# Performance work log

Hardware: AMD Instinct MI355X
Metric: run time of the kernel (lower is better)

## Reference

```python
import jax, jax.numpy as jnp
import numpy as np
from jax import lax

# ---- config (mirrors UpFIRDnConv2d(in=64,out=64,k=3,stride=1,jit=False), in_size=128) ----
B, C_IN, C_OUT, K = 8, 64, 64, 3
IN_SIZE = 128
LRELU_UP = 2          # lrelu_upsampling
FILTER_SIZE = 6
UP = 2                # up_factor = ceil(max(in,out)*2/in) = 2 (out_size == in_size)
DN = 2                # dn_factor = 2
GAIN = float(np.sqrt(2.0))
SLOPE = 0.2


def _firwin_lowpass(numtaps, cutoff, width, fs):
    """Replicates scipy.signal.firwin(numtaps, cutoff, width=width, fs=fs) for lowpass."""
    nyq = fs / 2.0
    c = cutoff / nyq            # normalized cutoff (~0.99995)
    w = width / nyq             # normalized transition width (2.0)
    # kaiser_atten / kaiser_beta (scipy formulas)
    atten = 2.285 * (numtaps - 1) * np.pi * w + 7.95
    if atten > 50:
        beta = 0.1102 * (atten - 8.7)
    elif atten > 21:
        beta = 0.5842 * (atten - 21) ** 0.4 + 0.07886 * (atten - 21)
    else:
        beta = 0.0
    m = np.arange(numtaps) - (numtaps - 1) / 2.0
    h = c * np.sinc(c * m) * np.kaiser(numtaps, beta)
    h = h / h.sum()             # scale=True at f=0
    return h.astype(np.float32)


def setup_inputs() -> dict:
    key = jax.random.key(0)
    k1, k2, k3 = jax.random.split(key, 3)
    x = jax.random.normal(k1, (B, C_IN, IN_SIZE, IN_SIZE), dtype=jnp.float32)
    # Conv2d(64,64,3) params (kaiming-ish scale: 1/sqrt(fan_in))
    fan_in = C_IN * K * K
    conv_w = jax.random.normal(k2, (C_OUT, C_IN, K, K), dtype=jnp.float32) / np.sqrt(fan_in)
    conv_b = jax.random.normal(k3, (C_OUT,), dtype=jnp.float32) * 0.01
    # UpFIRDn2d bias initialized to zeros (reset_parameters)
    bias = jnp.zeros((1, C_OUT, 1, 1), dtype=jnp.float32)
    # FIR filters from firwin (in_size == out_size == 128 here)
    uptaps = FILTER_SIZE * UP   # 12
    dntaps = FILTER_SIZE * DN   # 12
    up1d = _firwin_lowpass(uptaps, IN_SIZE / 2.0001, IN_SIZE, IN_SIZE)
    dn1d = _firwin_lowpass(dntaps, IN_SIZE / 2.0001, IN_SIZE, IN_SIZE)
    up_filter = jnp.asarray(np.outer(up1d, up1d)[None, None], dtype=jnp.float32)  # (1,1,12,12)
    dn_filter = jnp.asarray(np.outer(dn1d, dn1d)[None, None], dtype=jnp.float32)
    return {"x": x, "conv_w": conv_w, "conv_b": conv_b, "bias": bias,
            "up_filter": up_filter, "dn_filter": dn_filter}


def _conv_same(z, w):
    # torch padding='same': total = k-1, left = total//2, extra on the right
    kh, kw = w.shape[-2], w.shape[-1]
    lo_h, lo_w = (kh - 1) // 2, (kw - 1) // 2
    pad = [(lo_h, kh - 1 - lo_h), (lo_w, kw - 1 - lo_w)]
    return lax.conv_general_dilated(z, w, window_strides=(1, 1), padding=pad,
                                    dimension_numbers=("NCHW", "OIHW", "NCHW"))


def reference(x, conv_w, conv_b, bias, up_filter, dn_filter):
    # main 3x3 conv, stride 1, 'same'
    y = _conv_same(x, conv_w) + conv_b[None, :, None, None]
    # UpFIRDn2d
    y = y + bias                                   # (B, C, H, W)
    b, c, h, w = y.shape
    y = y.reshape(b * c, 1, h, w)
    y = jnp.repeat(jnp.repeat(y, UP, axis=2), UP, axis=3)   # nearest upsample -> (BC,1,2H,2W)
    y = _conv_same(y, up_filter)                   # 12x12 FIR, 'same'
    y = jnp.where(y >= 0, y, SLOPE * y) * jnp.float32(GAIN) # leaky_relu * gain
    y = _conv_same(y, dn_filter)                   # 12x12 FIR, 'same'
    y = y[:, :, ::DN, ::DN]                        # grid pool
    return y.reshape(b, c, y.shape[-2], y.shape[-1])
```

## Files before the change

kernel.cpp:

```cpp
#include <hip/hip_runtime.h>
#include <hip/hip_bf16.h>
#include <math.h>

#define NB 8
#define CH 64
#define IN_SZ 128
#define PLANE (IN_SZ*IN_SZ)

typedef __attribute__((ext_vector_type(8))) short short8;
typedef __attribute__((ext_vector_type(4))) float f32x4;
typedef __attribute__((ext_vector_type(4))) int   int4v;

#define Y0B   (NB*CH*PLANE*4)
#define WHB   (9*64*64*2)


__device__ __forceinline__ short8 dpp_shift_p1(short8 a, short8 nb) {
  int4v ai = __builtin_bit_cast(int4v, a);
  int4v ni = __builtin_bit_cast(int4v, nb);
  int4v r;
#pragma unroll
  for (int t = 0; t < 4; ++t) {
    int m = __builtin_amdgcn_update_dpp(0, ai[t], 0x101, 0xf, 0xf, true);
    int n = __builtin_amdgcn_update_dpp(0, ni[t], 0x11F, 0xf, 0xf, true);
    r[t] = m | n;
  }
  return __builtin_bit_cast(short8, r);
}
__device__ __forceinline__ short8 dpp_shift_m1(short8 a, short8 nb) {
  int4v ai = __builtin_bit_cast(int4v, a);
  int4v ni = __builtin_bit_cast(int4v, nb);
  int4v r;
#pragma unroll
  for (int t = 0; t < 4; ++t) {
    int m = __builtin_amdgcn_update_dpp(0, ai[t], 0x111, 0xf, 0xf, true);
    int n = __builtin_amdgcn_update_dpp(0, ni[t], 0x10F, 0xf, 0xf, true);
    r[t] = m | n;
  }
  return __builtin_bit_cast(short8, r);
}

__global__ __launch_bounds__(256) void prep_w_kernel(
    const float* __restrict__ w,
    const float* __restrict__ cb,
    const float* __restrict__ bias,
    const float* __restrict__ up2,
    const float* __restrict__ dn2,
    __hip_bfloat16* __restrict__ whi,
    __hip_bfloat16* __restrict__ wlo,
    float* __restrict__ bsum,
    float* __restrict__ f1d) {
  int t = blockIdx.x * 256 + threadIdx.x;
  if (t < 9*64*64) {
    int e   = t & 7;
    int l16 = (t >> 3) & 15;
    int g   = (t >> 7) & 3;
    int ct  = (t >> 9) & 3;
    int cih = (t >> 11) & 1;
    int tap = t >> 12;
    int co = ct*16 + l16;
    int ci = cih*32 + g*8 + e;
    int ky = tap / 3, kx = tap % 3;
    float v = w[((co*64 + ci)*3 + ky)*3 + kx];
    __hip_bfloat16 h = __float2bfloat16(v);
    whi[t] = h;
    wlo[t] = __float2bfloat16(v - __bfloat162float(h));
  }
  if (blockIdx.x == 0) {
    int tid = threadIdx.x;
    if (tid < 64) bsum[tid] = cb[tid] + bias[tid];
    float us = sqrtf(up2[5*12 + 5]);
    float ds = sqrtf(dn2[5*12 + 5]);
    if (tid >= 64 && tid < 70) {
      int j = tid - 64;
      f1d[j] = (up2[(2*j)*12 + 5] + up2[(2*j + 1)*12 + 5]) / us;
    } else if (tid >= 70 && tid < 77) {
      int j = tid - 70;
      float v;
      if (j == 0)      v = up2[0*12 + 5];
      else if (j == 6) v = up2[11*12 + 5];
      else             v = up2[(2*j - 1)*12 + 5] + up2[(2*j)*12 + 5];
      f1d[6 + j] = v / us;
    } else if (tid >= 77 && tid < 89) {
      int k = tid - 77;
      f1d[13 + k] = dn2[k*12 + 5] / ds;
    }
  }
}

__global__ __launch_bounds__(256) void prep_x_kernel(
    const float* __restrict__ x,
    __hip_bfloat16* __restrict__ xhi,
    __hip_bfloat16* __restrict__ xlo) {
  __shared__ float tile[64][129];
  int blk = blockIdx.x;
  int y = blk & 127;
  int b = blk >> 7;
  int tid = threadIdx.x;
  for (int i = 0; i < 32; ++i) {
    int idx = i*256 + tid;
    int ci = idx >> 7, xc = idx & 127;
    tile[ci][xc] = x[((size_t)(b*64 + ci)*128 + y)*128 + xc];
  }
  __syncthreads();
  unsigned* oh = (unsigned*)xhi;
  unsigned* ol = (unsigned*)xlo;
  size_t rowu = (size_t)(b*128 + y)*4096;
  for (int i = 0; i < 16; ++i) {
    int u = i*256 + tid;
    int ep  = u & 3;
    int l16 = (u >> 2) & 15;
    int g   = (u >> 6) & 3;
    int cih = (u >> 8) & 1;
    int xb  = u >> 9;
    int ci0 = cih*32 + g*8 + ep*2;
    int xc  = xb*16 + l16;
    float v0 = tile[ci0][xc];
    float v1 = tile[ci0 + 1][xc];
    __hip_bfloat16 h0 = __float2bfloat16(v0);
    __hip_bfloat16 h1 = __float2bfloat16(v1);
    __hip_bfloat16 l0 = __float2bfloat16(v0 - __bfloat162float(h0));
    __hip_bfloat16 l1 = __float2bfloat16(v1 - __bfloat162float(h1));
    unsigned uh = (unsigned)*(unsigned short*)&h0 | ((unsigned)*(unsigned short*)&h1 << 16);
    unsigned ul = (unsigned)*(unsigned short*)&l0 | ((unsigned)*(unsigned short*)&l1 << 16);
    oh[rowu + u] = uh;
    ol[rowu + u] = ul;
  }
}

__global__ __launch_bounds__(256, 3) void conv_mfma_kernel(
    const __hip_bfloat16* __restrict__ xhi,
    const __hip_bfloat16* __restrict__ xlo,
    const __hip_bfloat16* __restrict__ whi,
    const __hip_bfloat16* __restrict__ wlo,
    const float* __restrict__ bsum,
    float* __restrict__ y0) {
  int blk = blockIdx.x;
  int colq = blk & 3;
  int rg  = (blk >> 2) & 31;
  int b   = blk >> 7;
  int tid = threadIdx.x;
  int wv  = tid >> 6;
  int lane = tid & 63;
  int l16 = lane & 15;
  int g   = lane >> 4;
  int y   = rg*4 + wv;
  int xb  = colq*2;
  int px0 = colq*32;

  f32x4 acc[4][2];
#pragma unroll
  for (int ct = 0; ct < 4; ++ct) {
#pragma unroll
    for (int r = 0; r < 4; ++r) {
      float bv = bsum[ct*16 + g*4 + r];
#pragma unroll
      for (int pt = 0; pt < 2; ++pt) acc[ct][pt][r] = bv;
    }
  }

  const short8 zv8 = {0,0,0,0,0,0,0,0};
  int lofs = (g*16 + l16)*8;

  for (int dy = -1; dy <= 1; ++dy) {
    int ry = y + dy;
    if ((unsigned)ry >= 128u) continue;
    const __hip_bfloat16* rh = xhi + (size_t)(b*128 + ry)*8192;
    const __hip_bfloat16* rl = xlo + (size_t)(b*128 + ry)*8192;
#pragma unroll
    for (int cih = 0; cih < 2; ++cih) {
      short8 Fh[4], Fl[4];
#pragma unroll
      for (int i = 0; i < 4; ++i) {
        int xbF = xb - 1 + i;
        if ((unsigned)xbF < 8u) {
          size_t off = (size_t)((xbF*2 + cih)*64)*8 + lofs;
          Fh[i] = *(const short8*)(rh + off);
          Fl[i] = *(const short8*)(rl + off);
        } else {
          Fh[i] = zv8; Fl[i] = zv8;
        }
      }
#pragma unroll
      for (int dxn = 0; dxn < 3; ++dxn) {
        int tap = (dy + 1)*3 + dxn;
        short8 xhf[2], xlf[2];
#pragma unroll
        for (int pt = 0; pt < 2; ++pt) {
          if (dxn == 1) { xhf[pt] = Fh[pt + 1]; xlf[pt] = Fl[pt + 1]; }
          else if (dxn == 2) {
            xhf[pt] = dpp_shift_p1(Fh[pt + 1], Fh[pt + 2]);
            xlf[pt] = dpp_shift_p1(Fl[pt + 1], Fl[pt + 2]);
          } else {
            xhf[pt] = dpp_shift_m1(Fh[pt + 1], Fh[pt]);
            xlf[pt] = dpp_shift_m1(Fl[pt + 1], Fl[pt]);
          }
        }
        const __hip_bfloat16* wb = whi + (size_t)((tap*2 + cih)*4)*512;
        const __hip_bfloat16* wlb = wlo + (size_t)((tap*2 + cih)*4)*512;
#pragma unroll
        for (int ct = 0; ct < 4; ++ct) {
          short8 wh = *(const short8*)(wb  + (size_t)ct*512 + lofs);
          short8 wl = *(const short8*)(wlb + (size_t)ct*512 + lofs);
#pragma unroll
          for (int pt = 0; pt < 2; ++pt) {
            acc[ct][pt] = __builtin_amdgcn_mfma_f32_16x16x32_bf16(wh, xhf[pt], acc[ct][pt], 0, 0, 0);
            acc[ct][pt] = __builtin_amdgcn_mfma_f32_16x16x32_bf16(wl, xhf[pt], acc[ct][pt], 0, 0, 0);
            acc[ct][pt] = __builtin_amdgcn_mfma_f32_16x16x32_bf16(wh, xlf[pt], acc[ct][pt], 0, 0, 0);
          }
        }
      }
    }
  }

  float* yb = y0 + (size_t)b*64*PLANE + y*128 + px0;
#pragma unroll
  for (int ct = 0; ct < 4; ++ct)
#pragma unroll
    for (int pt = 0; pt < 2; ++pt)
#pragma unroll
      for (int r = 0; r < 4; ++r) {
        int co = ct*16 + g*4 + r;
        yb[(size_t)co*PLANE + pt*16 + l16] = acc[ct][pt][r];
      }
}

#define ZOFF  0
#define YOFF  0
#define HOFF  10360
#define DHOFF 10360
#define ZP 140
#define HP 140
#define YP 76
#define DHP 64

__global__ __launch_bounds__(512, 4) void upfirdn_kernel(
    const float* __restrict__ y0,
    const float* __restrict__ f1d,
    float* __restrict__ out) {
  __shared__ float lds[16380];

  int tid   = threadIdx.x;
  int blk   = blockIdx.x;
  int tile  = blk & 7;
  int plane = blk >> 3;
  int ty = tile >> 1, tx = tile & 1;
  int i0 = ty*32, j0 = tx*64;
  const float* yp = y0 + (size_t)plane*PLANE;

  float ef[6], of[7], dnf[12];
#pragma unroll
  for (int j = 0; j < 6; ++j) ef[j] = f1d[j];
#pragma unroll
  for (int j = 0; j < 7; ++j) of[j] = f1d[6 + j];
#pragma unroll
  for (int k = 0; k < 12; ++k) dnf[k] = f1d[13 + k];

  for (int p = tid; p < 43*76; p += 512) {
    int r = p / 76, c = p - r*76;
    int gy = i0 - 5 + r, gx = j0 - 5 + c;
    float v = 0.f;
    if (((unsigned)gy < 128u) && ((unsigned)gx < 128u)) v = yp[gy*IN_SZ + gx];
    lds[YOFF + r*YP + c] = v;
  }
  __syncthreads();

  for (int p = tid; p < 43*35; p += 512) {
    int m = p / 35, G = p - m*35;
    const float* yr = lds + YOFF + m*YP + 2*G;
    float4 ya = *(const float4*)(yr);
    float4 yb = *(const float4*)(yr + 4);
    float yreg[8] = {ya.x, ya.y, ya.z, ya.w, yb.x, yb.y, yb.z, yb.w};
    float hv[4];
#pragma unroll
    for (int s = 0; s < 4; ++s) {
      int base = s >> 1;
      float a = 0.f;
      if ((s & 1) == 0) {
#pragma unroll
        for (int j = 0; j < 6; ++j) a += ef[j]*yreg[base + j];
      } else {
#pragma unroll
        for (int j = 0; j < 7; ++j) a += of[j]*yreg[base + j];
      }
      hv[s] = a;
    }
    *(float4*)(lds + HOFF + m*HP + 4*G) = make_float4(hv[0], hv[1], hv[2], hv[3]);
  }
  __syncthreads();

  int Qy0 = 2*i0 - 5, Qx0 = 2*j0 - 5;
  for (int p = tid; p < 19*35; p += 512) {
    int gq = p / 35, q = p - gq*35;
    f32x4 hreg[8];
#pragma unroll
    for (int r = 0; r < 8; ++r) {
      int hrow = 2*gq + r;
      if (hrow > 42) hrow = 42;
      hreg[r] = *(const f32x4*)(lds + HOFF + hrow*HP + 4*q);
    }
    int qx0 = Qx0 + 4*q;
#pragma unroll
    for (int s = 0; s < 4; ++s) {
      int qyi = 4*gq + s;
      if (qyi < 74) {
        int base = s >> 1;
        f32x4 a = {0.f, 0.f, 0.f, 0.f};
        if ((s & 1) == 0) {
#pragma unroll
          for (int j = 0; j < 6; ++j) a += ef[j]*hreg[base + j];
        } else {
#pragma unroll
          for (int j = 0; j < 7; ++j) a += of[j]*hreg[base + j];
        }
        bool yok = (unsigned)(Qy0 + qyi) < 256u;
        f32x4 zv;
#pragma unroll
        for (int t = 0; t < 4; ++t) {
          float av = a[t];
          av = (av >= 0.f ? av : 0.2f*av) * 1.4142135623730951f;
          bool ok = yok && ((unsigned)(qx0 + t) < 256u);
          zv[t] = ok ? av : 0.f;
        }
        *(f32x4*)(lds + ZOFF + qyi*ZP + 4*q) = zv;
      }
    }
  }
  __syncthreads();

  for (int p = tid; p < 74*16; p += 512) {
    int qyi = p >> 4, gj = p & 15;
    const float* zr = lds + ZOFF + qyi*ZP + 8*gj;
    float4 z0 = *(const float4*)(zr);
    float4 z1 = *(const float4*)(zr + 4);
    float4 z2 = *(const float4*)(zr + 8);
    float4 z3 = *(const float4*)(zr + 12);
    float2 z4 = *(const float2*)(zr + 16);
    float zreg[18] = {z0.x,z0.y,z0.z,z0.w, z1.x,z1.y,z1.z,z1.w,
                      z2.x,z2.y,z2.z,z2.w, z3.x,z3.y,z3.z,z3.w, z4.x,z4.y};
    float dv[4];
#pragma unroll
    for (int s = 0; s < 4; ++s) {
      float a = 0.f;
#pragma unroll
      for (int k = 0; k < 12; ++k) a += dnf[k]*zreg[2*s + k];
      dv[s] = a;
    }
    *(float4*)(lds + DHOFF + qyi*DHP + 4*gj) = make_float4(dv[0], dv[1], dv[2], dv[3]);
  }
  __syncthreads();

  {
    int gi = tid >> 6, j = tid & 63;
    float dreg[18];
#pragma unroll
    for (int r = 0; r < 18; ++r) dreg[r] = lds[DHOFF + (8*gi + r)*DHP + j];
    float* op = out + (size_t)plane*PLANE + (i0 + 4*gi)*IN_SZ + (j0 + j);
#pragma unroll
    for (int s = 0; s < 4; ++s) {
      float a = 0.f;
#pragma unroll
      for (int k = 0; k < 12; ++k) a += dnf[k]*dreg[2*s + k];
      op[s*IN_SZ] = a;
    }
  }
}

extern "C" void kernel_launch(void* const* d_in, const int* in_sizes, int n_in,
                              void* d_out, int out_size, void* d_ws, size_t ws_size,
                              hipStream_t stream) {
  const float* x      = (const float*)d_in[0];
  const float* conv_w = (const float*)d_in[1];
  const float* conv_b = (const float*)d_in[2];
  const float* bias   = (const float*)d_in[3];
  const float* up2    = (const float*)d_in[4];
  const float* dn2    = (const float*)d_in[5];
  float* outp = (float*)d_out;

  char* ws = (char*)d_ws;
  float* y0  = (float*)(ws);
  __hip_bfloat16* whi = (__hip_bfloat16*)(ws + Y0B);
  __hip_bfloat16* wlo = (__hip_bfloat16*)(ws + Y0B + WHB);
  float* bsum = (float*)(ws + Y0B + 2*WHB);
  float* f1d  = (float*)(ws + Y0B + 2*WHB + 256);

  __hip_bfloat16* xhi = (__hip_bfloat16*)d_out;
  __hip_bfloat16* xlo = xhi + (size_t)NB*PLANE*64;

  prep_w_kernel<<<144, 256, 0, stream>>>(conv_w, conv_b, bias, up2, dn2, whi, wlo, bsum, f1d);
  prep_x_kernel<<<1024, 256, 0, stream>>>(x, xhi, xlo);
  conv_mfma_kernel<<<1024, 256, 0, stream>>>(xhi, xlo, whi, wlo, bsum, y0);
  upfirdn_kernel<<<4096, 512, 0, stream>>>(y0, f1d, outp);
}
```

Measured before the change: 192.6 us.

## Vectorize prep, compute two rows per conv wave, fuse upfirdn stages

Three separate changes. The x-prep kernel now uses 128-bit loads and stores. The MFMA conv kernel computes two output rows per wave so each weight fragment load feeds twice as many MFMAs, with half the blocks and a lower occupancy hint. The upfirdn kernel reorders the separable passes: it upsamples vertically first, then fuses horizontal upsample, leaky-relu and horizontal downsample in registers, which removes one LDS stage and one barrier and shrinks LDS use. The costs are higher register pressure in the conv kernel and fewer concurrent blocks.

```diff
diff --git a/kernel.cpp b/kernel.cpp
--- a/kernel.cpp
+++ b/kernel.cpp
@@ -10,6 +10,7 @@
 typedef __attribute__((ext_vector_type(8))) short short8;
 typedef __attribute__((ext_vector_type(4))) float f32x4;
 typedef __attribute__((ext_vector_type(4))) int   int4v;
+typedef __attribute__((ext_vector_type(4))) unsigned uint4v;
 
 #define Y0B   (NB*CH*PLANE*4)
 #define WHB   (9*64*64*2)
@@ -92,43 +93,50 @@
     const float* __restrict__ x,
     __hip_bfloat16* __restrict__ xhi,
     __hip_bfloat16* __restrict__ xlo) {
-  __shared__ float tile[64][129];
+  __shared__ float tile[64][132];
   int blk = blockIdx.x;
   int y = blk & 127;
   int b = blk >> 7;
   int tid = threadIdx.x;
-  for (int i = 0; i < 32; ++i) {
+#pragma unroll
+  for (int i = 0; i < 8; ++i) {
     int idx = i*256 + tid;
-    int ci = idx >> 7, xc = idx & 127;
-    tile[ci][xc] = x[((size_t)(b*64 + ci)*128 + y)*128 + xc];
+    int ci = idx >> 5, xf = idx & 31;
+    f32x4 v = *(const f32x4*)(x + ((size_t)(b*64 + ci)*128 + y)*128 + 4*xf);
+    *(f32x4*)(&tile[ci][4*xf]) = v;
   }
   __syncthreads();
-  unsigned* oh = (unsigned*)xhi;
-  unsigned* ol = (unsigned*)xlo;
-  size_t rowu = (size_t)(b*128 + y)*4096;
-  for (int i = 0; i < 16; ++i) {
+  uint4v* oh = (uint4v*)xhi;
+  uint4v* ol = (uint4v*)xlo;
+  size_t rowc = (size_t)(b*128 + y)*1024;
+#pragma unroll
+  for (int i = 0; i < 4; ++i) {
     int u = i*256 + tid;
-    int ep  = u & 3;
-    int l16 = (u >> 2) & 15;
-    int g   = (u >> 6) & 3;
-    int cih = (u >> 8) & 1;
-    int xb  = u >> 9;
-    int ci0 = cih*32 + g*8 + ep*2;
+    int l16 = u & 15;
+    int xb  = (u >> 4) & 7;
+    int cih = (u >> 7) & 1;
+    int g   = (u >> 8) & 3;
+    int ci0 = cih*32 + g*8;
     int xc  = xb*16 + l16;
-    float v0 = tile[ci0][xc];
-    float v1 = tile[ci0 + 1][xc];
-    __hip_bfloat16 h0 = __float2bfloat16(v0);
-    __hip_bfloat16 h1 = __float2bfloat16(v1);
-    __hip_bfloat16 l0 = __float2bfloat16(v0 - __bfloat162float(h0));
-    __hip_bfloat16 l1 = __float2bfloat16(v1 - __bfloat162float(h1));
-    unsigned uh = (unsigned)*(unsigned short*)&h0 | ((unsigned)*(unsigned short*)&h1 << 16);
-    unsigned ul = (unsigned)*(unsigned short*)&l0 | ((unsigned)*(unsigned short*)&l1 << 16);
-    oh[rowu + u] = uh;
-    ol[rowu + u] = ul;
-  }
-}
-
-__global__ __launch_bounds__(256, 3) void conv_mfma_kernel(
+    uint4v uh, ul;
+#pragma unroll
+    for (int ep = 0; ep < 4; ++ep) {
+      float v0 = tile[ci0 + 2*ep][xc];
+      float v1 = tile[ci0 + 2*ep + 1][xc];
+      __hip_bfloat16 h0 = __float2bfloat16(v0);
+      __hip_bfloat16 h1 = __float2bfloat16(v1);
+      __hip_bfloat16 l0 = __float2bfloat16(v0 - __bfloat162float(h0));
+      __hip_bfloat16 l1 = __float2bfloat16(v1 - __bfloat162float(h1));
+      uh[ep] = (unsigned)*(unsigned short*)&h0 | ((unsigned)*(unsigned short*)&h1 << 16);
+      ul[ep] = (unsigned)*(unsigned short*)&l0 | ((unsigned)*(unsigned short*)&l1 << 16);
+    }
+    size_t chunk = rowc + (size_t)(xb*128 + cih*64 + g*16 + l16);
+    oh[chunk] = uh;
+    ol[chunk] = ul;
+  }
+}
+
+__global__ __launch_bounds__(256, 2) void conv_mfma_kernel(
     const __hip_bfloat16* __restrict__ xhi,
     const __hip_bfloat16* __restrict__ xlo,
     const __hip_bfloat16* __restrict__ whi,
@@ -137,108 +145,119 @@
     float* __restrict__ y0) {
   int blk = blockIdx.x;
   int colq = blk & 3;
-  int rg  = (blk >> 2) & 31;
-  int b   = blk >> 7;
+  int rg  = (blk >> 2) & 15;
+  int b   = blk >> 6;
   int tid = threadIdx.x;
   int wv  = tid >> 6;
   int lane = tid & 63;
   int l16 = lane & 15;
   int g   = lane >> 4;
-  int y   = rg*4 + wv;
+  int yr0 = rg*8 + wv*2;
   int xb  = colq*2;
   int px0 = colq*32;
 
-  f32x4 acc[4][2];
+  f32x4 acc[2][4][2];
 #pragma unroll
   for (int ct = 0; ct < 4; ++ct) {
 #pragma unroll
     for (int r = 0; r < 4; ++r) {
       float bv = bsum[ct*16 + g*4 + r];
 #pragma unroll
-      for (int pt = 0; pt < 2; ++pt) acc[ct][pt][r] = bv;
+      for (int rr = 0; rr < 2; ++rr)
+#pragma unroll
+        for (int pt = 0; pt < 2; ++pt) acc[rr][ct][pt][r] = bv;
     }
   }
 
   const short8 zv8 = {0,0,0,0,0,0,0,0};
   int lofs = (g*16 + l16)*8;
 
-  for (int dy = -1; dy <= 1; ++dy) {
-    int ry = y + dy;
-    if ((unsigned)ry >= 128u) continue;
-    const __hip_bfloat16* rh = xhi + (size_t)(b*128 + ry)*8192;
-    const __hip_bfloat16* rl = xlo + (size_t)(b*128 + ry)*8192;
-#pragma unroll
-    for (int cih = 0; cih < 2; ++cih) {
-      short8 Fh[4], Fl[4];
-#pragma unroll
-      for (int i = 0; i < 4; ++i) {
-        int xbF = xb - 1 + i;
-        if ((unsigned)xbF < 8u) {
-          size_t off = (size_t)((xbF*2 + cih)*64)*8 + lofs;
-          Fh[i] = *(const short8*)(rh + off);
-          Fl[i] = *(const short8*)(rl + off);
-        } else {
-          Fh[i] = zv8; Fl[i] = zv8;
+#pragma unroll
+  for (int cih = 0; cih < 2; ++cih) {
+    for (int dy = -1; dy <= 1; ++dy) {
+      short8 Fh[2][4], Fl[2][4];
+#pragma unroll
+      for (int rr = 0; rr < 2; ++rr) {
+        int ry = yr0 + rr + dy;
+        bool rok = (unsigned)ry < 128u;
+        const __hip_bfloat16* rh = xhi + (size_t)(b*128 + ry)*8192;
+        const __hip_bfloat16* rl = xlo + (size_t)(b*128 + ry)*8192;
+#pragma unroll
+        for (int i = 0; i < 4; ++i) {
+          int xbF = xb - 1 + i;
+          bool ok = rok && ((unsigned)xbF < 8u);
+          if (ok) {
+            size_t off = (size_t)((xbF*2 + cih)*64)*8 + lofs;
+            Fh[rr][i] = *(const short8*)(rh + off);
+            Fl[rr][i] = *(const short8*)(rl + off);
+          } else {
+            Fh[rr][i] = zv8; Fl[rr][i] = zv8;
+          }
         }
       }
 #pragma unroll
       for (int dxn = 0; dxn < 3; ++dxn) {
         int tap = (dy + 1)*3 + dxn;
-        short8 xhf[2], xlf[2];
-#pragma unroll
-        for (int pt = 0; pt < 2; ++pt) {
-          if (dxn == 1) { xhf[pt] = Fh[pt + 1]; xlf[pt] = Fl[pt + 1]; }
-          else if (dxn == 2) {
-            xhf[pt] = dpp_shift_p1(Fh[pt + 1], Fh[pt + 2]);
-            xlf[pt] = dpp_shift_p1(Fl[pt + 1], Fl[pt + 2]);
-          } else {
-            xhf[pt] = dpp_shift_m1(Fh[pt + 1], Fh[pt]);
-            xlf[pt] = dpp_shift_m1(Fl[pt + 1], Fl[pt]);
+        short8 xh[2][2], xl[2][2];
+#pragma unroll
+        for (int rr = 0; rr < 2; ++rr)
+#pragma unroll
+          for (int pt = 0; pt < 2; ++pt) {
+            if (dxn == 1) { xh[rr][pt] = Fh[rr][pt + 1]; xl[rr][pt] = Fl[rr][pt + 1]; }
+            else if (dxn == 2) {
+              xh[rr][pt] = dpp_shift_p1(Fh[rr][pt + 1], Fh[rr][pt + 2]);
+              xl[rr][pt] = dpp_shift_p1(Fl[rr][pt + 1], Fl[rr][pt + 2]);
+            } else {
+              xh[rr][pt] = dpp_shift_m1(Fh[rr][pt + 1], Fh[rr][pt]);
+              xl[rr][pt] = dpp_shift_m1(Fl[rr][pt + 1], Fl[rr][pt]);
+            }
           }
-        }
-        const __hip_bfloat16* wb = whi + (size_t)((tap*2 + cih)*4)*512;
+        const __hip_bfloat16* wb  = whi + (size_t)((tap*2 + cih)*4)*512;
         const __hip_bfloat16* wlb = wlo + (size_t)((tap*2 + cih)*4)*512;
 #pragma unroll
         for (int ct = 0; ct < 4; ++ct) {
           short8 wh = *(const short8*)(wb  + (size_t)ct*512 + lofs);
           short8 wl = *(const short8*)(wlb + (size_t)ct*512 + lofs);
 #pragma unroll
-          for (int pt = 0; pt < 2; ++pt) {
-            acc[ct][pt] = __builtin_amdgcn_mfma_f32_16x16x32_bf16(wh, xhf[pt], acc[ct][pt], 0, 0, 0);
-            acc[ct][pt] = __builtin_amdgcn_mfma_f32_16x16x32_bf16(wl, xhf[pt], acc[ct][pt], 0, 0, 0);
-            acc[ct][pt] = __builtin_amdgcn_mfma_f32_16x16x32_bf16(wh, xlf[pt], acc[ct][pt], 0, 0, 0);
-          }
+          for (int rr = 0; rr < 2; ++rr)
+#pragma unroll
+            for (int pt = 0; pt < 2; ++pt) {
+              acc[rr][ct][pt] = __builtin_amdgcn_mfma_f32_16x16x32_bf16(wh, xh[rr][pt], acc[rr][ct][pt], 0, 0, 0);
+              acc[rr][ct][pt] = __builtin_amdgcn_mfma_f32_16x16x32_bf16(wl, xh[rr][pt], acc[rr][ct][pt], 0, 0, 0);
+              acc[rr][ct][pt] = __builtin_amdgcn_mfma_f32_16x16x32_bf16(wh, xl[rr][pt], acc[rr][ct][pt], 0, 0, 0);
+            }
         }
       }
     }
   }
 
-  float* yb = y0 + (size_t)b*64*PLANE + y*128 + px0;
-#pragma unroll
-  for (int ct = 0; ct < 4; ++ct)
-#pragma unroll
-    for (int pt = 0; pt < 2; ++pt)
-#pragma unroll
-      for (int r = 0; r < 4; ++r) {
-        int co = ct*16 + g*4 + r;
-        yb[(size_t)co*PLANE + pt*16 + l16] = acc[ct][pt][r];
-      }
-}
-
-#define ZOFF  0
+#pragma unroll
+  for (int rr = 0; rr < 2; ++rr) {
+    float* yb = y0 + (size_t)b*64*PLANE + (yr0 + rr)*128 + px0;
+#pragma unroll
+    for (int ct = 0; ct < 4; ++ct)
+#pragma unroll
+      for (int pt = 0; pt < 2; ++pt)
+#pragma unroll
+        for (int r = 0; r < 4; ++r) {
+          int co = ct*16 + g*4 + r;
+          yb[(size_t)co*PLANE + pt*16 + l16] = acc[rr][ct][pt][r];
+        }
+  }
+}
+
 #define YOFF  0
-#define HOFF  10360
-#define DHOFF 10360
-#define ZP 140
-#define HP 140
-#define YP 76
-#define DHP 64
+#define DHOFF 0
+#define HVOFF 5032
+#define YP  76
+#define HVP 76
+#define DHP 68
 
 __global__ __launch_bounds__(512, 4) void upfirdn_kernel(
     const float* __restrict__ y0,
     const float* __restrict__ f1d,
     float* __restrict__ out) {
-  __shared__ float lds[16380];
+  __shared__ float lds[10656];
 
   int tid   = threadIdx.x;
   int blk   = blockIdx.x;
@@ -265,88 +284,79 @@
   }
   __syncthreads();
 
-  for (int p = tid; p < 43*35; p += 512) {
-    int m = p / 35, G = p - m*35;
-    const float* yr = lds + YOFF + m*YP + 2*G;
-    float4 ya = *(const float4*)(yr);
-    float4 yb = *(const float4*)(yr + 4);
-    float yreg[8] = {ya.x, ya.y, ya.z, ya.w, yb.x, yb.y, yb.z, yb.w};
-    float hv[4];
+  if (tid < 361) {
+    int g = tid / 19, cq = tid - (tid / 19)*19;
+    f32x4 yv[8];
+#pragma unroll
+    for (int r = 0; r < 8; ++r) {
+      int row = 2*g + r;
+      if (row > 42) row = 42;
+      yv[r] = *(const f32x4*)(lds + YOFF + row*YP + 4*cq);
+    }
 #pragma unroll
     for (int s = 0; s < 4; ++s) {
-      int base = s >> 1;
-      float a = 0.f;
-      if ((s & 1) == 0) {
-#pragma unroll
-        for (int j = 0; j < 6; ++j) a += ef[j]*yreg[base + j];
-      } else {
-#pragma unroll
-        for (int j = 0; j < 7; ++j) a += of[j]*yreg[base + j];
-      }
-      hv[s] = a;
-    }
-    *(float4*)(lds + HOFF + m*HP + 4*G) = make_float4(hv[0], hv[1], hv[2], hv[3]);
-  }
-  __syncthreads();
-
-  int Qy0 = 2*i0 - 5, Qx0 = 2*j0 - 5;
-  for (int p = tid; p < 19*35; p += 512) {
-    int gq = p / 35, q = p - gq*35;
-    f32x4 hreg[8];
-#pragma unroll
-    for (int r = 0; r < 8; ++r) {
-      int hrow = 2*gq + r;
-      if (hrow > 42) hrow = 42;
-      hreg[r] = *(const f32x4*)(lds + HOFF + hrow*HP + 4*q);
-    }
-    int qx0 = Qx0 + 4*q;
-#pragma unroll
-    for (int s = 0; s < 4; ++s) {
-      int qyi = 4*gq + s;
+      int qyi = 4*g + s;
       if (qyi < 74) {
-        int base = s >> 1;
+        int bb = s >> 1;
         f32x4 a = {0.f, 0.f, 0.f, 0.f};
         if ((s & 1) == 0) {
 #pragma unroll
-          for (int j = 0; j < 6; ++j) a += ef[j]*hreg[base + j];
+          for (int j = 0; j < 6; ++j) a += ef[j]*yv[bb + j];
         } else {
 #pragma unroll
-          for (int j = 0; j < 7; ++j) a += of[j]*hreg[base + j];
-        }
-        bool yok = (unsigned)(Qy0 + qyi) < 256u;
-        f32x4 zv;
-#pragma unroll
-        for (int t = 0; t < 4; ++t) {
-          float av = a[t];
-          av = (av >= 0.f ? av : 0.2f*av) * 1.4142135623730951f;
-          bool ok = yok && ((unsigned)(qx0 + t) < 256u);
-          zv[t] = ok ? av : 0.f;
-        }
-        *(f32x4*)(lds + ZOFF + qyi*ZP + 4*q) = zv;
+          for (int j = 0; j < 7; ++j) a += of[j]*yv[bb + j];
+        }
+        *(f32x4*)(lds + HVOFF + qyi*HVP + 4*cq) = a;
       }
     }
   }
   __syncthreads();
 
-  for (int p = tid; p < 74*16; p += 512) {
-    int qyi = p >> 4, gj = p & 15;
-    const float* zr = lds + ZOFF + qyi*ZP + 8*gj;
-    float4 z0 = *(const float4*)(zr);
-    float4 z1 = *(const float4*)(zr + 4);
-    float4 z2 = *(const float4*)(zr + 8);
-    float4 z3 = *(const float4*)(zr + 12);
-    float2 z4 = *(const float2*)(zr + 16);
-    float zreg[18] = {z0.x,z0.y,z0.z,z0.w, z1.x,z1.y,z1.z,z1.w,
-                      z2.x,z2.y,z2.z,z2.w, z3.x,z3.y,z3.z,z3.w, z4.x,z4.y};
-    float dv[4];
-#pragma unroll
-    for (int s = 0; s < 4; ++s) {
-      float a = 0.f;
-#pragma unroll
-      for (int k = 0; k < 12; ++k) a += dnf[k]*zreg[2*s + k];
-      dv[s] = a;
-    }
-    *(float4*)(lds + DHOFF + qyi*DHP + 4*gj) = make_float4(dv[0], dv[1], dv[2], dv[3]);
+  {
+    int Qy0 = 2*i0 - 5, Qx0 = 2*j0 - 5;
+    for (int p = tid; p < 74*8; p += 512) {
+      int qyi = p >> 3, jg = p & 7;
+      float* dhp = lds + DHOFF + qyi*DHP + 8*jg;
+      int qy = Qy0 + qyi;
+      if ((unsigned)qy >= 256u) {
+        f32x4 zz = {0.f, 0.f, 0.f, 0.f};
+        *(f32x4*)dhp = zz;
+        *(f32x4*)(dhp + 4) = zz;
+      } else {
+        float hv[20];
+        const float* hp = lds + HVOFF + qyi*HVP + 8*jg;
+#pragma unroll
+        for (int i = 0; i < 5; ++i) *(f32x4*)(hv + 4*i) = *(const f32x4*)(hp + 4*i);
+        int qxb = Qx0 + 16*jg;
+        float z[26];
+#pragma unroll
+        for (int m = 0; m < 26; ++m) {
+          int t = m >> 1;
+          float a = 0.f;
+          if ((m & 1) == 0) {
+#pragma unroll
+            for (int j = 0; j < 6; ++j) a += ef[j]*hv[t + j];
+          } else {
+#pragma unroll
+            for (int j = 0; j < 7; ++j) a += of[j]*hv[t + j];
+          }
+          a = (a >= 0.f ? a : 0.2f*a) * 1.4142135623730951f;
+          z[m] = ((unsigned)(qxb + m) < 256u) ? a : 0.f;
+        }
+        float dv[8];
+#pragma unroll
+        for (int d = 0; d < 8; ++d) {
+          float a = 0.f;
+#pragma unroll
+          for (int k = 0; k < 12; ++k) a += dnf[k]*z[2*d + k];
+          dv[d] = a;
+        }
+        f32x4 o0 = {dv[0], dv[1], dv[2], dv[3]};
+        f32x4 o1 = {dv[4], dv[5], dv[6], dv[7]};
+        *(f32x4*)dhp = o0;
+        *(f32x4*)(dhp + 4) = o1;
+      }
+    }
   }
   __syncthreads();
 
@@ -389,6 +399,6 @@
 
   prep_w_kernel<<<144, 256, 0, stream>>>(conv_w, conv_b, bias, up2, dn2, whi, wlo, bsum, f1d);
   prep_x_kernel<<<1024, 256, 0, stream>>>(x, xhi, xlo);
-  conv_mfma_kernel<<<1024, 256, 0, stream>>>(xhi, xlo, whi, wlo, bsum, y0);
+  conv_mfma_kernel<<<512, 256, 0, stream>>>(xhi, xlo, whi, wlo, bsum, y0);
   upfirdn_kernel<<<4096, 512, 0, stream>>>(y0, f1d, outp);
 }
```

After: 186.5 us. 3.1% less time.
